# Kernel optimization log

Hardware: AMD Instinct MI355X
Metric: run time of the kernel (lower is better)

The kernel has to match this reference:

```python
import jax, jax.numpy as jnp
import numpy as np

V_TH = 1.0
V_RESET = 0.0
BN_EPS = 1e-5

# Heaviside spike with ATan surrogate gradient (spikingjelly surrogate.ATan, alpha=2)
@jax.custom_vjp
def spike(x):
    return (x >= 0).astype(x.dtype)

def _spike_fwd(x):
    return spike(x), x

def _spike_bwd(x, g):
    alpha = 2.0
    sg = (alpha / 2.0) / (1.0 + (jnp.pi / 2.0 * alpha * x) ** 2)
    return (g * sg,)

spike.defvjp(_spike_fwd, _spike_bwd)


def lif_block(x, w, W, b, gamma, beta):
    """LTLIF (learnable tau, decay_input=False, hard reset) -> Linear -> BatchNorm1d.
    x: [T, B, C]"""
    inv_tau = jax.nn.sigmoid(w)  # 1/tau, learnable via w

    def step(v, xt):
        # decay_input=False charge: v = v - (v - v_reset)/tau + x_t
        v = v - (v - V_RESET) * inv_tau + xt
        s = spike(v - V_TH)
        v = (1.0 - s) * v + s * V_RESET  # hard reset
        return v, s

    v0 = jnp.full(x.shape[1:], V_RESET, dtype=x.dtype)
    _, spikes = jax.lax.scan(step, v0, x)  # spikes: [T, B, C]

    y = jnp.einsum('tbc,dc->tbd', spikes, W) + b  # Linear per step
    # BatchNorm1d in multi-step mode: stats over flattened (T*B) per channel
    mean = jnp.mean(y, axis=(0, 1))
    var = jnp.var(y, axis=(0, 1))
    y = (y - mean) * jax.lax.rsqrt(var + BN_EPS) * gamma + beta
    return y


def setup_inputs() -> dict:
    key = jax.random.key(0)
    ks = jax.random.split(key, 3)
    T, B, C = 128, 256, 512
    scale = 1.0 / np.sqrt(C)
    return {
        'x': jax.random.normal(ks[0], (T, B, C), jnp.float32),
        'w0': jnp.zeros((), jnp.float32),  # sigmoid(0)=0.5 => tau=2
        'W0': jax.random.normal(ks[1], (C, C), jnp.float32) * scale,
        'b0': jnp.zeros((C,), jnp.float32),
        'gamma0': jnp.ones((C,), jnp.float32),
        'beta0': jnp.zeros((C,), jnp.float32),
        'w1': jnp.zeros((), jnp.float32),
        'W1': jax.random.normal(ks[2], (C, C), jnp.float32) * scale,
        'b1': jnp.zeros((C,), jnp.float32),
        'gamma1': jnp.ones((C,), jnp.float32),
        'beta1': jnp.zeros((C,), jnp.float32),
    }


def reference(x, w0, W0, b0, gamma0, beta0, w1, W1, b1, gamma1, beta1):
    h = lif_block(x, w0, W0, b0, gamma0, beta0)   # process block (Dropout p=0 -> identity)
    h = lif_block(h, w1, W1, b1, gamma1, beta1)   # out block
    return h + x  # skip_connect=True
```

## Files before the change

kernel.cpp:

```cpp
#include <hip/hip_runtime.h>


typedef int i32x4 __attribute__((ext_vector_type(4)));

#define T_STEPS 128
#define BATCH   256
#define CH      512
#define BC      (BATCH * CH)
#define MROWS   (T_STEPS * BATCH)

__device__ __forceinline__ void llds16(const void* g, void* l) {
  __builtin_amdgcn_global_load_lds(
      (const __attribute__((address_space(1))) void*)g,
      (__attribute__((address_space(3))) void*)l, 16, 0, 0);
}

__global__ __launch_bounds__(256) void k_convw(const float* __restrict__ W,
                                               signed char* __restrict__ WL) {
  int i = blockIdx.x * 256 + threadIdx.x;
  double z = (double)W[i] * 4294967296.0;
  z = fmin(fmax(z, -2147483647.0), 2147483647.0);
  int q = (int)llrint(z);
  int r = q;
  signed char l0 = (signed char)r; r = (r - l0) >> 8;
  signed char l1 = (signed char)r; r = (r - l1) >> 8;
  signed char l2 = (signed char)r; r = (r - l2) >> 8;
  signed char l3 = (signed char)r;
  WL[i]          = l0;
  WL[i + 262144] = l1;
  WL[i + 524288] = l2;
  WL[i + 786432] = l3;
}

__global__ __launch_bounds__(256) void k_lif1(const float* __restrict__ X,
                                              const float* __restrict__ wp,
                                              signed char* __restrict__ S) {
  int i4 = blockIdx.x * 256 + threadIdx.x;
  float inv_tau = 1.0f / (1.0f + expf(-wp[0]));
  float om = 1.0f - inv_tau;
  float v0 = 0.f, v1 = 0.f, v2 = 0.f, v3 = 0.f;
  for (int t = 0; t < T_STEPS; ++t) {
    float4 x = ((const float4*)X)[(size_t)t * (BC / 4) + i4];
    char4 s;
    v0 = v0 * om + x.x; s.x = (v0 >= 1.f); v0 = s.x ? 0.f : v0;
    v1 = v1 * om + x.y; s.y = (v1 >= 1.f); v1 = s.y ? 0.f : v1;
    v2 = v2 * om + x.z; s.z = (v2 >= 1.f); v2 = s.z ? 0.f : v2;
    v3 = v3 * om + x.w; s.w = (v3 >= 1.f); v3 = s.w ? 0.f : v3;
    ((char4*)S)[(size_t)t * (BC / 4) + i4] = s;
  }
}

__global__ __launch_bounds__(256) void k_lif2(const float* __restrict__ Y,
                                              const double* __restrict__ sA,
                                              const double* __restrict__ sB,
                                              const float* __restrict__ wp,
                                              signed char* __restrict__ S) {
  int i4 = blockIdx.x * 256 + threadIdx.x;
  int c0 = (i4 * 4) & (CH - 1);
  double a0 = sA[c0], a1 = sA[c0 + 1], a2 = sA[c0 + 2], a3 = sA[c0 + 3];
  double b0 = sB[c0], b1 = sB[c0 + 1], b2 = sB[c0 + 2], b3 = sB[c0 + 3];
  float inv_tau = 1.0f / (1.0f + expf(-wp[0]));
  float om = 1.0f - inv_tau;
  float v0 = 0.f, v1 = 0.f, v2 = 0.f, v3 = 0.f;
  for (int t = 0; t < T_STEPS; ++t) {
    float4 y = ((const float4*)Y)[(size_t)t * (BC / 4) + i4];
    char4 s;
    float h0 = (float)((double)y.x * a0 + b0);
    float h1 = (float)((double)y.y * a1 + b1);
    float h2 = (float)((double)y.z * a2 + b2);
    float h3 = (float)((double)y.w * a3 + b3);
    v0 = v0 * om + h0; s.x = (v0 >= 1.f); v0 = s.x ? 0.f : v0;
    v1 = v1 * om + h1; s.y = (v1 >= 1.f); v1 = s.y ? 0.f : v1;
    v2 = v2 * om + h2; s.z = (v2 >= 1.f); v2 = s.z ? 0.f : v2;
    v3 = v3 * om + h3; s.w = (v3 >= 1.f); v3 = s.w ? 0.f : v3;
    ((char4*)S)[(size_t)t * (BC / 4) + i4] = s;
  }
}

__global__ __launch_bounds__(256) void k_gemm(const signed char* __restrict__ S,
                                              const signed char* __restrict__ WL,
                                              float* __restrict__ Y,
                                              double* __restrict__ sumP,
                                              double* __restrict__ sqP) {
  __shared__ __align__(16) signed char Ab[2][128 * 64];
  __shared__ __align__(16) signed char Bb[2][4][64 * 64];

  const int tid  = threadIdx.x;
  const int wid  = tid >> 6;
  const int lane = tid & 63;
  const int bid   = blockIdx.x;
  const int xcd   = bid & 7;
  const int local = bid >> 3;
  const int bn    = local & 7;
  const int bm    = xcd * 32 + (local >> 3);
  const int m0 = bm * 128, n0 = bn * 64;
  const int wm = wid >> 1, wn = wid & 1;

  i32x4 acc[4][2][4] = {};

  auto STAGE = [&](int buf, int kt) {
    #pragma unroll
    for (int p = 0; p < 2; ++p) {
      int cid = p * 256 + tid, row = cid >> 2, gl = cid & 3;
      int gg = gl ^ ((row >> 1) & 3);
      llds16(S + (size_t)(m0 + row) * 512 + kt + gg * 16,
             (char*)Ab[buf] + p * 4096 + wid * 1024);
    }
    #pragma unroll
    for (int j = 0; j < 4; ++j) {
      int row = tid >> 2, gl = tid & 3;
      int gg = gl ^ ((row >> 1) & 3);
      llds16(WL + (size_t)j * 262144 + (size_t)(n0 + row) * 512 + kt + gg * 16,
             (char*)Bb[buf][j] + wid * 1024);
    }
  };

  STAGE(0, 0);
  #pragma unroll
  for (int i = 0; i < 8; ++i) {
    const int cur = i & 1;
    if (i < 7) STAGE(cur ^ 1, (i + 1) * 64);

    if (i < 7) asm volatile("s_waitcnt vmcnt(6)" ::: "memory");
    else       asm volatile("s_waitcnt vmcnt(0)" ::: "memory");
    __builtin_amdgcn_s_barrier();
    asm volatile("" ::: "memory");

    i32x4 a[4];
    #pragma unroll
    for (int m = 0; m < 4; ++m) {
      int r = wm * 64 + m * 16 + (lane & 15);
      int g = (lane >> 4) ^ ((r >> 1) & 3);
      a[m] = *(const i32x4*)(Ab[cur] + r * 64 + g * 16);
    }
    #pragma unroll
    for (int j = 0; j < 4; ++j) {
      i32x4 b[2];
      #pragma unroll
      for (int n = 0; n < 2; ++n) {
        int r = wn * 32 + n * 16 + (lane & 15);
        int g = (lane >> 4) ^ ((r >> 1) & 3);
        b[n] = *(const i32x4*)(Bb[cur][j] + r * 64 + g * 16);
      }
      #pragma unroll
      for (int m = 0; m < 4; ++m)
        #pragma unroll
        for (int n = 0; n < 2; ++n)
          acc[m][n][j] = __builtin_amdgcn_mfma_i32_16x16x64_i8(
              a[m], b[n], acc[m][n][j], 0, 0, 0);
    }

    asm volatile("s_waitcnt lgkmcnt(0)" ::: "memory");
    __builtin_amdgcn_s_barrier();
  }

  const int r0 = m0 + wm * 64 + (lane >> 4) * 4;
  const int cl = wn * 32 + (lane & 15);
  double s0 = 0, q0 = 0, s1 = 0, q1 = 0;
  #pragma unroll
  for (int m = 0; m < 4; ++m)
    #pragma unroll
    for (int n = 0; n < 2; ++n)
      #pragma unroll
      for (int q = 0; q < 4; ++q) {
        double yv = (((double)acc[m][n][3][q] * 256.0 + (double)acc[m][n][2][q]) * 256.0
                     + (double)acc[m][n][1][q]) * 256.0 + (double)acc[m][n][0][q];
        float yf = (float)(yv * 0x1p-32);
        Y[(size_t)(r0 + m * 16 + q) * 512 + n0 + cl + n * 16] = yf;
        double yd = (double)yf;
        if (n == 0) { s0 += yd; q0 += yd * yd; }
        else        { s1 += yd; q1 += yd * yd; }
      }
  s0 += __shfl_xor(s0, 16); s0 += __shfl_xor(s0, 32);
  q0 += __shfl_xor(q0, 16); q0 += __shfl_xor(q0, 32);
  s1 += __shfl_xor(s1, 16); s1 += __shfl_xor(s1, 32);
  q1 += __shfl_xor(q1, 16); q1 += __shfl_xor(q1, 32);

  double* shS = (double*)Ab[0];
  double* shQ = shS + 128;
  if (lane < 16) {
    shS[wm * 64 + cl]      = s0;  shQ[wm * 64 + cl]      = q0;
    shS[wm * 64 + cl + 16] = s1;  shQ[wm * 64 + cl + 16] = q1;
  }
  __syncthreads();
  if (tid < 64) {
    sumP[(size_t)(n0 + tid) * 256 + bm] = shS[tid] + shS[64 + tid];
    sqP [(size_t)(n0 + tid) * 256 + bm] = shQ[tid] + shQ[64 + tid];
  }
}

__global__ __launch_bounds__(256) void k_stats2(const double* __restrict__ sumP,
                                                const double* __restrict__ sqP,
                                                const float* __restrict__ gamma,
                                                const float* __restrict__ beta,
                                                double* __restrict__ sA,
                                                double* __restrict__ sB) {
  __shared__ double shS[256], shQ[256];
  int c = blockIdx.x;
  int t = threadIdx.x;
  shS[t] = sumP[(size_t)c * 256 + t];
  shQ[t] = sqP [(size_t)c * 256 + t];
  __syncthreads();
  for (int w = 128; w >= 1; w >>= 1) {
    if (t < w) { shS[t] += shS[t + w]; shQ[t] += shQ[t + w]; }
    __syncthreads();
  }
  if (t == 0) {
    const double invN = 1.0 / 32768.0;
    double mean = shS[0] * invN;
    double var  = shQ[0] * invN - mean * mean;
    double rstd = rsqrt(var + 1e-5);
    double a = (double)gamma[c] * rstd;
    sA[c] = a;
    sB[c] = (double)beta[c] - mean * a;
  }
}

__global__ __launch_bounds__(256) void k_final(float* __restrict__ Y,
                                               const float* __restrict__ X,
                                               const double* __restrict__ sA,
                                               const double* __restrict__ sB) {
  size_t i = (size_t)blockIdx.x * 256 + threadIdx.x;
  int c0 = (int)((i * 4) & (CH - 1));
  float4 y = ((const float4*)Y)[i];
  float4 x = ((const float4*)X)[i];
  float4 o;
  o.x = (float)((double)y.x * sA[c0 + 0] + sB[c0 + 0] + (double)x.x);
  o.y = (float)((double)y.y * sA[c0 + 1] + sB[c0 + 1] + (double)x.y);
  o.z = (float)((double)y.z * sA[c0 + 2] + sB[c0 + 2] + (double)x.z);
  o.w = (float)((double)y.w * sA[c0 + 3] + sB[c0 + 3] + (double)x.w);
  ((float4*)Y)[i] = o;
}

extern "C" void kernel_launch(void* const* d_in, const int* in_sizes, int n_in,
                              void* d_out, int out_size, void* d_ws, size_t ws_size,
                              hipStream_t stream) {
  (void)in_sizes; (void)n_in; (void)out_size; (void)ws_size;

  const float* x   = (const float*)d_in[0];
  const float* w0  = (const float*)d_in[1];
  const float* W0  = (const float*)d_in[2];
  const float* g0  = (const float*)d_in[4];
  const float* be0 = (const float*)d_in[5];
  const float* w1  = (const float*)d_in[6];
  const float* W1  = (const float*)d_in[7];
  const float* g1  = (const float*)d_in[9];
  const float* be1 = (const float*)d_in[10];
  float* Y = (float*)d_out;

  char* ws = (char*)d_ws;
  signed char* WL0  = (signed char*)(ws + 0x0000000);
  signed char* WL1  = (signed char*)(ws + 0x0100000);
  signed char* spk  = (signed char*)(ws + 0x0200000);
  double*      sumP = (double*)(ws + 0x1200000);
  double*      sqP  = (double*)(ws + 0x1300000);
  double*      sA   = (double*)(ws + 0x1400000);
  double*      sB   = (double*)(ws + 0x1402000);

  k_convw<<<1024, 256, 0, stream>>>(W0, WL0);
  k_convw<<<1024, 256, 0, stream>>>(W1, WL1);

  k_lif1 <<<BC / 4 / 256, 256, 0, stream>>>(x, w0, spk);
  k_gemm <<<(MROWS / 128) * (CH / 64), 256, 0, stream>>>(spk, WL0, Y, sumP, sqP);
  k_stats2<<<512, 256, 0, stream>>>(sumP, sqP, g0, be0, sA, sB);

  k_lif2 <<<BC / 4 / 256, 256, 0, stream>>>(Y, sA, sB, w1, spk);
  k_gemm <<<(MROWS / 128) * (CH / 64), 256, 0, stream>>>(spk, WL1, Y, sumP, sqP);
  k_stats2<<<512, 256, 0, stream>>>(sumP, sqP, g1, be1, sA, sB);

  k_final<<<(MROWS * CH) / (4 * 256), 256, 0, stream>>>(Y, x, sA, sB);
}
```

Before: 210.2 us.

## Load GEMM A fragments directly to registers, merge weight conversion, scalarize LIF kernels

The GEMM no longer stages the spike (A) tile through LDS. Each wave loads its A fragments straight from global memory into double-buffered registers, which frees LDS and drops the A shared-memory reads. Only B goes through LDS, with the MFMA loop bracketed by sched_barrier and setprio. The two weight-conversion launches become one launch, and the LIF kernels switch from float4 per thread in 256-thread blocks to one element per thread in 64-thread blocks, trading wider loads for many more independent waves to hide latency.

```diff
diff --git a/kernel.cpp b/kernel.cpp
--- a/kernel.cpp
+++ b/kernel.cpp
@@ -15,9 +15,14 @@
       (__attribute__((address_space(3))) void*)l, 16, 0, 0);
 }
 
-__global__ __launch_bounds__(256) void k_convw(const float* __restrict__ W,
-                                               signed char* __restrict__ WL) {
-  int i = blockIdx.x * 256 + threadIdx.x;
+__global__ __launch_bounds__(256) void k_convw(const float* __restrict__ W0,
+                                               const float* __restrict__ W1,
+                                               signed char* __restrict__ WL0,
+                                               signed char* __restrict__ WL1) {
+  int b = blockIdx.x;
+  const float* W = (b < 1024) ? W0 : W1;
+  signed char* WL = (b < 1024) ? WL0 : WL1;
+  int i = (b & 1023) * 256 + threadIdx.x;
   double z = (double)W[i] * 4294967296.0;
   z = fmin(fmax(z, -2147483647.0), 2147483647.0);
   int q = (int)llrint(z);
@@ -32,48 +37,39 @@
   WL[i + 786432] = l3;
 }
 
-__global__ __launch_bounds__(256) void k_lif1(const float* __restrict__ X,
-                                              const float* __restrict__ wp,
-                                              signed char* __restrict__ S) {
-  int i4 = blockIdx.x * 256 + threadIdx.x;
-  float inv_tau = 1.0f / (1.0f + expf(-wp[0]));
-  float om = 1.0f - inv_tau;
-  float v0 = 0.f, v1 = 0.f, v2 = 0.f, v3 = 0.f;
+__global__ __launch_bounds__(64) void k_lif1(const float* __restrict__ X,
+                                             const float* __restrict__ wp,
+                                             signed char* __restrict__ S) {
+  int i = blockIdx.x * 64 + threadIdx.x;
+  float om = 1.0f - 1.0f / (1.0f + expf(-wp[0]));
+  float v = 0.0f;
+  #pragma unroll 8
   for (int t = 0; t < T_STEPS; ++t) {
-    float4 x = ((const float4*)X)[(size_t)t * (BC / 4) + i4];
-    char4 s;
-    v0 = v0 * om + x.x; s.x = (v0 >= 1.f); v0 = s.x ? 0.f : v0;
-    v1 = v1 * om + x.y; s.y = (v1 >= 1.f); v1 = s.y ? 0.f : v1;
-    v2 = v2 * om + x.z; s.z = (v2 >= 1.f); v2 = s.z ? 0.f : v2;
-    v3 = v3 * om + x.w; s.w = (v3 >= 1.f); v3 = s.w ? 0.f : v3;
-    ((char4*)S)[(size_t)t * (BC / 4) + i4] = s;
-  }
-}
-
-__global__ __launch_bounds__(256) void k_lif2(const float* __restrict__ Y,
-                                              const double* __restrict__ sA,
-                                              const double* __restrict__ sB,
-                                              const float* __restrict__ wp,
-                                              signed char* __restrict__ S) {
-  int i4 = blockIdx.x * 256 + threadIdx.x;
-  int c0 = (i4 * 4) & (CH - 1);
-  double a0 = sA[c0], a1 = sA[c0 + 1], a2 = sA[c0 + 2], a3 = sA[c0 + 3];
-  double b0 = sB[c0], b1 = sB[c0 + 1], b2 = sB[c0 + 2], b3 = sB[c0 + 3];
-  float inv_tau = 1.0f / (1.0f + expf(-wp[0]));
-  float om = 1.0f - inv_tau;
-  float v0 = 0.f, v1 = 0.f, v2 = 0.f, v3 = 0.f;
+    float xt = X[(size_t)t * BC + i];
+    v = v * om + xt;
+    bool sp = (v >= 1.0f);
+    S[(size_t)t * BC + i] = sp;
+    v = sp ? 0.0f : v;
+  }
+}
+
+__global__ __launch_bounds__(64) void k_lif2(const float* __restrict__ Y,
+                                             const double* __restrict__ sA,
+                                             const double* __restrict__ sB,
+                                             const float* __restrict__ wp,
+                                             signed char* __restrict__ S) {
+  int i = blockIdx.x * 64 + threadIdx.x;
+  int c = i & (CH - 1);
+  double a = sA[c], b = sB[c];
+  float om = 1.0f - 1.0f / (1.0f + expf(-wp[0]));
+  float v = 0.0f;
+  #pragma unroll 8
   for (int t = 0; t < T_STEPS; ++t) {
-    float4 y = ((const float4*)Y)[(size_t)t * (BC / 4) + i4];
-    char4 s;
-    float h0 = (float)((double)y.x * a0 + b0);
-    float h1 = (float)((double)y.y * a1 + b1);
-    float h2 = (float)((double)y.z * a2 + b2);
-    float h3 = (float)((double)y.w * a3 + b3);
-    v0 = v0 * om + h0; s.x = (v0 >= 1.f); v0 = s.x ? 0.f : v0;
-    v1 = v1 * om + h1; s.y = (v1 >= 1.f); v1 = s.y ? 0.f : v1;
-    v2 = v2 * om + h2; s.z = (v2 >= 1.f); v2 = s.z ? 0.f : v2;
-    v3 = v3 * om + h3; s.w = (v3 >= 1.f); v3 = s.w ? 0.f : v3;
-    ((char4*)S)[(size_t)t * (BC / 4) + i4] = s;
+    float h = (float)((double)Y[(size_t)t * BC + i] * a + b);
+    v = v * om + h;
+    bool sp = (v >= 1.0f);
+    S[(size_t)t * BC + i] = sp;
+    v = sp ? 0.0f : v;
   }
 }
 
@@ -82,7 +78,6 @@
                                               float* __restrict__ Y,
                                               double* __restrict__ sumP,
                                               double* __restrict__ sqP) {
-  __shared__ __align__(16) signed char Ab[2][128 * 64];
   __shared__ __align__(16) signed char Bb[2][4][64 * 64];
 
   const int tid  = threadIdx.x;
@@ -95,67 +90,69 @@
   const int bm    = xcd * 32 + (local >> 3);
   const int m0 = bm * 128, n0 = bn * 64;
   const int wm = wid >> 1, wn = wid & 1;
+  const int lr = lane & 15, lg = lane >> 4;
 
   i32x4 acc[4][2][4] = {};
 
   auto STAGE = [&](int buf, int kt) {
-    #pragma unroll
-    for (int p = 0; p < 2; ++p) {
-      int cid = p * 256 + tid, row = cid >> 2, gl = cid & 3;
-      int gg = gl ^ ((row >> 1) & 3);
-      llds16(S + (size_t)(m0 + row) * 512 + kt + gg * 16,
-             (char*)Ab[buf] + p * 4096 + wid * 1024);
-    }
-    #pragma unroll
-    for (int j = 0; j < 4; ++j) {
-      int row = tid >> 2, gl = tid & 3;
-      int gg = gl ^ ((row >> 1) & 3);
+    int row = tid >> 2, gl = tid & 3;
+    int gg = gl ^ ((row >> 1) & 3);
+    #pragma unroll
+    for (int j = 0; j < 4; ++j)
       llds16(WL + (size_t)j * 262144 + (size_t)(n0 + row) * 512 + kt + gg * 16,
              (char*)Bb[buf][j] + wid * 1024);
-    }
   };
 
+  const signed char* aP = S + (size_t)(m0 + wm * 64 + lr) * 512 + lg * 16;
+  i32x4 a[2][4];
+
   STAGE(0, 0);
+  #pragma unroll
+  for (int m = 0; m < 4; ++m)
+    a[0][m] = *(const i32x4*)(aP + m * 8192);
+
   #pragma unroll
   for (int i = 0; i < 8; ++i) {
     const int cur = i & 1;
-    if (i < 7) STAGE(cur ^ 1, (i + 1) * 64);
-
-    if (i < 7) asm volatile("s_waitcnt vmcnt(6)" ::: "memory");
+    if (i < 7) {
+      STAGE(cur ^ 1, (i + 1) * 64);
+      #pragma unroll
+      for (int m = 0; m < 4; ++m)
+        a[cur ^ 1][m] = *(const i32x4*)(aP + m * 8192 + (i + 1) * 64);
+    }
+    if (i < 7) asm volatile("s_waitcnt vmcnt(8)" ::: "memory");
     else       asm volatile("s_waitcnt vmcnt(0)" ::: "memory");
     __builtin_amdgcn_s_barrier();
     asm volatile("" ::: "memory");
 
-    i32x4 a[4];
-    #pragma unroll
-    for (int m = 0; m < 4; ++m) {
-      int r = wm * 64 + m * 16 + (lane & 15);
-      int g = (lane >> 4) ^ ((r >> 1) & 3);
-      a[m] = *(const i32x4*)(Ab[cur] + r * 64 + g * 16);
+    i32x4 b[2][4];
+    #pragma unroll
+    for (int n = 0; n < 2; ++n) {
+      int r = wn * 32 + n * 16 + lr;
+      int g = lg ^ ((r >> 1) & 3);
+      #pragma unroll
+      for (int j = 0; j < 4; ++j)
+        b[n][j] = *(const i32x4*)(Bb[cur][j] + r * 64 + g * 16);
     }
-    #pragma unroll
-    for (int j = 0; j < 4; ++j) {
-      i32x4 b[2];
-      #pragma unroll
-      for (int n = 0; n < 2; ++n) {
-        int r = wn * 32 + n * 16 + (lane & 15);
-        int g = (lane >> 4) ^ ((r >> 1) & 3);
-        b[n] = *(const i32x4*)(Bb[cur][j] + r * 64 + g * 16);
-      }
+    __builtin_amdgcn_sched_barrier(0);
+
+    __builtin_amdgcn_s_setprio(1);
+    #pragma unroll
+    for (int j = 0; j < 4; ++j)
       #pragma unroll
       for (int m = 0; m < 4; ++m)
         #pragma unroll
         for (int n = 0; n < 2; ++n)
           acc[m][n][j] = __builtin_amdgcn_mfma_i32_16x16x64_i8(
-              a[m], b[n], acc[m][n][j], 0, 0, 0);
-    }
+              a[cur][m], b[n][j], acc[m][n][j], 0, 0, 0);
+    __builtin_amdgcn_s_setprio(0);
 
     asm volatile("s_waitcnt lgkmcnt(0)" ::: "memory");
     __builtin_amdgcn_s_barrier();
   }
 
-  const int r0 = m0 + wm * 64 + (lane >> 4) * 4;
-  const int cl = wn * 32 + (lane & 15);
+  const int r0 = m0 + wm * 64 + lg * 4;
+  const int cl = wn * 32 + lr;
   double s0 = 0, q0 = 0, s1 = 0, q1 = 0;
   #pragma unroll
   for (int m = 0; m < 4; ++m)
@@ -176,7 +173,7 @@
   s1 += __shfl_xor(s1, 16); s1 += __shfl_xor(s1, 32);
   q1 += __shfl_xor(q1, 16); q1 += __shfl_xor(q1, 32);
 
-  double* shS = (double*)Ab[0];
+  double* shS = (double*)Bb[0][0];
   double* shQ = shS + 128;
   if (lane < 16) {
     shS[wm * 64 + cl]      = s0;  shQ[wm * 64 + cl]      = q0;
@@ -257,14 +254,13 @@
   double*      sA   = (double*)(ws + 0x1400000);
   double*      sB   = (double*)(ws + 0x1402000);
 
-  k_convw<<<1024, 256, 0, stream>>>(W0, WL0);
-  k_convw<<<1024, 256, 0, stream>>>(W1, WL1);
-
-  k_lif1 <<<BC / 4 / 256, 256, 0, stream>>>(x, w0, spk);
+  k_convw<<<2048, 256, 0, stream>>>(W0, W1, WL0, WL1);
+
+  k_lif1 <<<BC / 64, 64, 0, stream>>>(x, w0, spk);
   k_gemm <<<(MROWS / 128) * (CH / 64), 256, 0, stream>>>(spk, WL0, Y, sumP, sqP);
   k_stats2<<<512, 256, 0, stream>>>(sumP, sqP, g0, be0, sA, sB);
 
-  k_lif2 <<<BC / 4 / 256, 256, 0, stream>>>(Y, sA, sB, w1, spk);
+  k_lif2 <<<BC / 64, 64, 0, stream>>>(Y, sA, sB, w1, spk);
   k_gemm <<<(MROWS / 128) * (CH / 64), 256, 0, stream>>>(spk, WL1, Y, sumP, sqP);
   k_stats2<<<512, 256, 0, stream>>>(sumP, sqP, g1, be1, sA, sB);
 
```

After: 217.5 us. +3.5%, slower.
